# Kernel tuning notes

Hardware: AMD Instinct MI355X
Metric: run time of the kernel (lower is better)

## Reference

```python
import jax, jax.numpy as jnp
import numpy as np

N_REL = 32
N_ATTR = 8
WIDTH = 256
N_ENT = 2048


def setup_inputs() -> dict:
    key = jax.random.key(0)
    k1, k2, k3 = jax.random.split(key, 3)
    database = jax.random.uniform(k1, (N_REL, N_ENT, N_ENT), dtype=jnp.float32)
    attributes = jax.random.uniform(k2, (N_ATTR, N_ENT), dtype=jnp.float32)
    weights = jax.random.normal(k3, (2 * N_REL + N_ATTR, WIDTH), dtype=jnp.float32)
    return {"database": database, "attributes": attributes, "weights": weights}


def reference(database, attributes, weights):
    # per-relation reductions over each entity dim: [R, N] each
    q = jnp.concatenate([
        database.sum(axis=1),          # sum over dim 1 -> [R, N]
        database.sum(axis=2),          # sum over dim 2 -> [R, N]
        attributes * 2.0,              # [A, N]
    ], axis=0)                          # [2R + A, N]
    quantified = 1.0 - jnp.exp(-q)
    # softmax over rows of weights (axis 0), then [W, 2R+A] @ [2R+A, N]
    w = jax.nn.softmax(weights, axis=0)
    outputs = jnp.einsum('kw,kn->wn', w, quantified)  # [WIDTH, N]
    return outputs, quantified
```

## Files before the change

kernel.cpp:

```cpp
#include <hip/hip_runtime.h>
#include <math.h>

#define NREL  32
#define NENT  2048
#define NATTR 8
#define WIDTH 256
#define NK    (2 * NREL + NATTR)
#define CHUNKS_OUT 16
#define SUBS  4

typedef float f4 __attribute__((ext_vector_type(4)));

__global__ __launch_bounds__(256) void reduce_db_kernel(
    const float* __restrict__ db,
    float* __restrict__ qout,
    float* __restrict__ partial,
    int rowsPerWave,
    int nSubs)
{
    const int bx   = blockIdx.x;
    const int r    = bx >> 4;
    const int cOut = bx & (CHUNKS_OUT - 1);
    const int tid  = threadIdx.x;
    const int wave = tid >> 6;
    const int lane = tid & 63;

    __shared__ __align__(16) float smem[4][NENT];
    float (*rpart)[33] = reinterpret_cast<float(*)[33]>(&smem[0][0]);

    const size_t rowStride = NENT / 4;
    const f4* relBase = reinterpret_cast<const f4*>(db)
                      + (size_t)r * NENT * rowStride
                      + (size_t)(cOut * 128) * rowStride
                      + lane;

    f4 acc[8];
#pragma unroll
    for (int k = 0; k < 8; ++k) acc[k] = (f4)0.f;

    for (int sc = 0; sc < nSubs; ++sc) {
        const int i0 = sc * 32;
        const f4* base = relBase
                       + (size_t)(i0 + wave * rowsPerWave) * rowStride;

        for (int j = 0; j < rowsPerWave; j += 2) {
            const f4* rowA = base + (size_t)j * rowStride;
            const f4* rowB = rowA + rowStride;
            float rsA = 0.f, rsB = 0.f;
#pragma unroll
            for (int k = 0; k < 8; ++k) {
                f4 v = __builtin_nontemporal_load(rowA + k * 64);
                acc[k] += v;
                rsA += (v.x + v.y) + (v.z + v.w);
            }
#pragma unroll
            for (int k = 0; k < 8; ++k) {
                f4 v = __builtin_nontemporal_load(rowB + k * 64);
                acc[k] += v;
                rsB += (v.x + v.y) + (v.z + v.w);
            }
            rpart[lane][wave * rowsPerWave + j]     = rsA;
            rpart[lane][wave * rowsPerWave + j + 1] = rsB;
        }
        __syncthreads();

        {
            const int row = tid >> 3;
            const int seg = tid & 7;
            float t = 0.f;
#pragma unroll
            for (int i = 0; i < 8; ++i) t += rpart[seg * 8 + i][row];
            t += __shfl_xor(t, 1, 64);
            t += __shfl_xor(t, 2, 64);
            t += __shfl_xor(t, 4, 64);
            if (seg == 0)
                qout[(size_t)(NREL + r) * NENT + cOut * 128 + i0 + row] =
                    1.f - __expf(-t);
        }
        __syncthreads();
    }

#pragma unroll
    for (int k = 0; k < 8; ++k)
        *reinterpret_cast<f4*>(&smem[wave][k * 256 + lane * 4]) = acc[k];
    __syncthreads();

    f4* part4 = reinterpret_cast<f4*>(partial) + (size_t)bx * rowStride;
    for (int g = tid; g < NENT / 4; g += 256) {
        f4 a0 = *reinterpret_cast<const f4*>(&smem[0][g * 4]);
        f4 a1 = *reinterpret_cast<const f4*>(&smem[1][g * 4]);
        f4 a2 = *reinterpret_cast<const f4*>(&smem[2][g * 4]);
        f4 a3 = *reinterpret_cast<const f4*>(&smem[3][g * 4]);
        part4[g] = (a0 + a1) + (a2 + a3);
    }
}

#define FIN_BLOCKS ((NREL + NATTR) * NENT / 256)

__global__ __launch_bounds__(256) void finalize_softmax_kernel(
    const float* __restrict__ partial,
    const float* __restrict__ attrs,
    const float* __restrict__ W,
    float* __restrict__ qout,
    float* __restrict__ sw)
{
    const int b = blockIdx.x;
    if (b < FIN_BLOCKS) {
        const int idx = b * 256 + threadIdx.x;
        const int row = idx >> 11;
        const int n   = idx & (NENT - 1);
        if (row < NREL) {
            float s = 0.f;
#pragma unroll
            for (int c = 0; c < CHUNKS_OUT; ++c)
                s += partial[((size_t)(row * CHUNKS_OUT + c) << 11) + n];
            qout[((size_t)row << 11) + n] = 1.f - __expf(-s);
        } else {
            const int a = row - NREL;
            float v = attrs[((size_t)a << 11) + n];
            qout[((size_t)(2 * NREL + a) << 11) + n] = 1.f - __expf(-2.f * v);
        }
    } else {
        const int w = threadIdx.x;
        float v[NK];
#pragma unroll
        for (int k = 0; k < NK; ++k) v[k] = W[k * WIDTH + w];
        float m = v[0];
#pragma unroll
        for (int k = 1; k < NK; ++k) m = fmaxf(m, v[k]);
        float s = 0.f;
#pragma unroll
        for (int k = 0; k < NK; ++k) { v[k] = __expf(v[k] - m); s += v[k]; }
        const float inv = 1.f / s;
#pragma unroll
        for (int k = 0; k < NK; ++k) sw[k * WIDTH + w] = v[k] * inv;
    }
}

#define CW   32
#define CCOL 128

__global__ __launch_bounds__(256) void matmul_kernel(
    const float* __restrict__ sw,
    const float* __restrict__ quant,
    float* __restrict__ out)
{
    __shared__ float qt[NK][CCOL];
    __shared__ float swt[NK][CW];
    const int wg  = blockIdx.x >> 4;
    const int cg  = blockIdx.x & 15;
    const int w0  = wg * CW;
    const int c0  = cg * CCOL;
    const int tid = threadIdx.x;

    const f4* q4 = reinterpret_cast<const f4*>(quant);
#pragma unroll
    for (int i = tid; i < NK * (CCOL / 4); i += 256) {
        const int k = i >> 5;
        const int c = i & 31;
        *reinterpret_cast<f4*>(&qt[k][c * 4]) =
            q4[(size_t)k * (NENT / 4) + (c0 >> 2) + c];
    }
#pragma unroll
    for (int i = tid; i < NK * CW; i += 256) {
        const int k  = i >> 5;
        const int wl = i & 31;
        swt[k][wl] = sw[k * WIDTH + w0 + wl];
    }
    __syncthreads();

    const int wl = tid >> 3;
    const int cl = (tid & 7) * 16;
    f4 a0 = (f4)0.f, a1 = (f4)0.f, a2 = (f4)0.f, a3 = (f4)0.f;
#pragma unroll 8
    for (int k = 0; k < NK; ++k) {
        const float s = swt[k][wl];
        const f4* row = reinterpret_cast<const f4*>(&qt[k][cl]);
        f4 v0 = row[0], v1 = row[1], v2 = row[2], v3 = row[3];
        a0 += s * v0; a1 += s * v1; a2 += s * v2; a3 += s * v3;
    }
    f4* o4 = reinterpret_cast<f4*>(out + (size_t)(w0 + wl) * NENT + c0 + cl);
    o4[0] = a0; o4[1] = a1; o4[2] = a2; o4[3] = a3;
}

extern "C" void kernel_launch(void* const* d_in, const int* in_sizes, int n_in,
                              void* d_out, int out_size, void* d_ws, size_t ws_size,
                              hipStream_t stream)
{
    const float* db    = (const float*)d_in[0];
    const float* attrs = (const float*)d_in[1];
    const float* W     = (const float*)d_in[2];

    float* out   = (float*)d_out;
    float* quant = out + (size_t)WIDTH * NENT;

    float* partial = (float*)d_ws;
    float* sw      = partial + (size_t)NREL * CHUNKS_OUT * NENT;

    reduce_db_kernel<<<NREL * CHUNKS_OUT, 256, 0, stream>>>(
        db, quant, partial, 8, SUBS);
    finalize_softmax_kernel<<<FIN_BLOCKS + 1, 256, 0, stream>>>(
        partial, attrs, W, quant, sw);
    matmul_kernel<<<(WIDTH / CW) * (NENT / CCOL), 256, 0, stream>>>(
        sw, quant, out);
}
```

Measured before the change: 100.2 us.

## Fuse finalize, softmax and matmul into a single tail kernel

Merges the finalize/softmax kernel and the matmul kernel into one launch. Matmul blocks recompute the column-sum finalization from the partial buffer, read the row-sum quantified values written by the reduce kernel, and compute the softmax weights per thread inline. Separate blocks still write the finalized quantified rows to the output. This drops one kernel launch and the round trip through the softmax workspace, at the cost of recomputing the partial sums, exp, and per-thread softmax in every matmul block.

```diff
diff --git a/kernel.cpp b/kernel.cpp
--- a/kernel.cpp
+++ b/kernel.cpp
@@ -95,18 +95,79 @@
     }
 }
 
+#define MM_BLOCKS  (NENT / 64)
 #define FIN_BLOCKS ((NREL + NATTR) * NENT / 256)
 
-__global__ __launch_bounds__(256) void finalize_softmax_kernel(
+__global__ __launch_bounds__(256) void tail_kernel(
     const float* __restrict__ partial,
     const float* __restrict__ attrs,
     const float* __restrict__ W,
     float* __restrict__ qout,
-    float* __restrict__ sw)
+    float* __restrict__ out)
 {
-    const int b = blockIdx.x;
-    if (b < FIN_BLOCKS) {
-        const int idx = b * 256 + threadIdx.x;
+    const int b   = blockIdx.x;
+    const int tid = threadIdx.x;
+
+    if (b < MM_BLOCKS) {
+        __shared__ __align__(16) float qt[NK][68];
+        const int c0  = b * 64;
+        const int cq  = c0 >> 2;
+        const f4* part4  = reinterpret_cast<const f4*>(partial);
+        const f4* qout4  = reinterpret_cast<const f4*>(qout);
+        const f4* attrs4 = reinterpret_cast<const f4*>(attrs);
+
+        for (int s = tid; s < 32 * 16; s += 256) {
+            const int row = s >> 4;
+            const int cf  = s & 15;
+            f4 sum = (f4)0.f;
+#pragma unroll
+            for (int c = 0; c < CHUNKS_OUT; ++c)
+                sum += part4[(size_t)(row * CHUNKS_OUT + c) * 512 + cq + cf];
+            f4 q;
+            q.x = 1.f - __expf(-sum.x); q.y = 1.f - __expf(-sum.y);
+            q.z = 1.f - __expf(-sum.z); q.w = 1.f - __expf(-sum.w);
+            *reinterpret_cast<f4*>(&qt[row][cf * 4]) = q;
+        }
+        for (int s = tid; s < 32 * 16; s += 256) {
+            const int row = s >> 4;
+            const int cf  = s & 15;
+            *reinterpret_cast<f4*>(&qt[32 + row][cf * 4]) =
+                qout4[(size_t)(32 + row) * 512 + cq + cf];
+        }
+        if (tid < 8 * 16) {
+            const int row = tid >> 4;
+            const int cf  = tid & 15;
+            f4 v = attrs4[(size_t)row * 512 + cq + cf];
+            f4 q;
+            q.x = 1.f - __expf(-2.f * v.x); q.y = 1.f - __expf(-2.f * v.y);
+            q.z = 1.f - __expf(-2.f * v.z); q.w = 1.f - __expf(-2.f * v.w);
+            *reinterpret_cast<f4*>(&qt[64 + row][cf * 4]) = q;
+        }
+        __syncthreads();
+
+        const int w = tid;
+        float m = W[w];
+#pragma unroll
+        for (int k = 1; k < NK; ++k) m = fmaxf(m, W[k * WIDTH + w]);
+        float ssum = 0.f;
+#pragma unroll
+        for (int k = 0; k < NK; ++k) ssum += __expf(W[k * WIDTH + w] - m);
+        const float inv = 1.f / ssum;
+
+        f4 acc[16];
+#pragma unroll
+        for (int i = 0; i < 16; ++i) acc[i] = (f4)0.f;
+        for (int k = 0; k < NK; ++k) {
+            const float s = __expf(W[k * WIDTH + w] - m) * inv;
+            const f4* qrow = reinterpret_cast<const f4*>(&qt[k][0]);
+#pragma unroll
+            for (int i = 0; i < 16; ++i) acc[i] += s * qrow[i];
+        }
+        f4* o4 = reinterpret_cast<f4*>(out + (size_t)w * NENT + c0);
+#pragma unroll
+        for (int i = 0; i < 16; ++i) o4[i] = acc[i];
+    } else {
+        const int idx = (b - MM_BLOCKS) * 256 + tid;
         const int row = idx >> 11;
         const int n   = idx & (NENT - 1);
         if (row < NREL) {
@@ -120,67 +181,7 @@
             float v = attrs[((size_t)a << 11) + n];
             qout[((size_t)(2 * NREL + a) << 11) + n] = 1.f - __expf(-2.f * v);
         }
-    } else {
-        const int w = threadIdx.x;
-        float v[NK];
-#pragma unroll
-        for (int k = 0; k < NK; ++k) v[k] = W[k * WIDTH + w];
-        float m = v[0];
-#pragma unroll
-        for (int k = 1; k < NK; ++k) m = fmaxf(m, v[k]);
-        float s = 0.f;
-#pragma unroll
-        for (int k = 0; k < NK; ++k) { v[k] = __expf(v[k] - m); s += v[k]; }
-        const float inv = 1.f / s;
-#pragma unroll
-        for (int k = 0; k < NK; ++k) sw[k * WIDTH + w] = v[k] * inv;
     }
-}
-
-#define CW   32
-#define CCOL 128
-
-__global__ __launch_bounds__(256) void matmul_kernel(
-    const float* __restrict__ sw,
-    const float* __restrict__ quant,
-    float* __restrict__ out)
-{
-    __shared__ float qt[NK][CCOL];
-    __shared__ float swt[NK][CW];
-    const int wg  = blockIdx.x >> 4;
-    const int cg  = blockIdx.x & 15;
-    const int w0  = wg * CW;
-    const int c0  = cg * CCOL;
-    const int tid = threadIdx.x;
-
-    const f4* q4 = reinterpret_cast<const f4*>(quant);
-#pragma unroll
-    for (int i = tid; i < NK * (CCOL / 4); i += 256) {
-        const int k = i >> 5;
-        const int c = i & 31;
-        *reinterpret_cast<f4*>(&qt[k][c * 4]) =
-            q4[(size_t)k * (NENT / 4) + (c0 >> 2) + c];
-    }
-#pragma unroll
-    for (int i = tid; i < NK * CW; i += 256) {
-        const int k  = i >> 5;
-        const int wl = i & 31;
-        swt[k][wl] = sw[k * WIDTH + w0 + wl];
-    }
-    __syncthreads();
-
-    const int wl = tid >> 3;
-    const int cl = (tid & 7) * 16;
-    f4 a0 = (f4)0.f, a1 = (f4)0.f, a2 = (f4)0.f, a3 = (f4)0.f;
-#pragma unroll 8
-    for (int k = 0; k < NK; ++k) {
-        const float s = swt[k][wl];
-        const f4* row = reinterpret_cast<const f4*>(&qt[k][cl]);
-        f4 v0 = row[0], v1 = row[1], v2 = row[2], v3 = row[3];
-        a0 += s * v0; a1 += s * v1; a2 += s * v2; a3 += s * v3;
-    }
-    f4* o4 = reinterpret_cast<f4*>(out + (size_t)(w0 + wl) * NENT + c0 + cl);
-    o4[0] = a0; o4[1] = a1; o4[2] = a2; o4[3] = a3;
 }
 
 extern "C" void kernel_launch(void* const* d_in, const int* in_sizes, int n_in,
@@ -195,12 +196,9 @@
     float* quant = out + (size_t)WIDTH * NENT;
 
     float* partial = (float*)d_ws;
-    float* sw      = partial + (size_t)NREL * CHUNKS_OUT * NENT;
 
     reduce_db_kernel<<<NREL * CHUNKS_OUT, 256, 0, stream>>>(
         db, quant, partial, 8, SUBS);
-    finalize_softmax_kernel<<<FIN_BLOCKS + 1, 256, 0, stream>>>(
-        partial, attrs, W, quant, sw);
-    matmul_kernel<<<(WIDTH / CW) * (NENT / CCOL), 256, 0, stream>>>(
-        sw, quant, out);
+    tail_kernel<<<MM_BLOCKS + FIN_BLOCKS, 256, 0, stream>>>(
+        partial, attrs, W, quant, out);
 }
```

After: 116.8 us. 16.5% more time.
